# Kernel tuning notes

Measured on AMD Instinct MI355X. Metric: run time of the kernel, lower is better.

Reference implementation:

```python
import jax, jax.numpy as jnp
import numpy as np

N = 1024       # sentence length (words incl. root at index 0)
WD = 300       # word embedding dim (GloVe-style)
PD = 25        # pos_emb_dim
H = 125        # hidden_dim_lstm
FC = 100       # hidden_dim_fc
PVOCAB = 50    # POS tagset size


def setup_inputs() -> dict:
    key = jax.random.key(0)
    ks = jax.random.split(key, 14)
    f = lambda k, s: jax.random.normal(k, s, dtype=jnp.float32) * 0.1
    d_in = WD + PD
    return {
        "word_vecs": jax.random.normal(ks[0], (N, WD), dtype=jnp.float32),
        "pos_idx": jax.random.randint(ks[1], (N,), 0, PVOCAB),
        "parents_ids": jax.random.randint(ks[2], (N,), 0, N),
        "pos_emb": f(ks[3], (PVOCAB, PD)),
        "Wih0": f(ks[4], (2, 4 * H, d_in)),
        "Whh0": f(ks[5], (2, 4 * H, H)),
        "b0": f(ks[6], (2, 4 * H)),
        "Wih1": f(ks[7], (2, 4 * H, 2 * H)),
        "Whh1": f(ks[8], (2, 4 * H, H)),
        "b1": f(ks[9], (2, 4 * H)),
        "fc1_W": f(ks[10], (FC, 4 * H)),
        "fc1_b": f(ks[11], (FC,)),
        "fc2_W": f(ks[12], (1, FC)),
        "fc2_b": f(ks[13], (1,)),
    }


def _lstm_dir(x, Wih, Whh, b, reverse):
    # torch LSTM cell, gate order (i, f, g, o); b = b_ih + b_hh
    Hd = Whh.shape[1]
    def step(carry, xt):
        h, c = carry
        g = xt @ Wih.T + h @ Whh.T + b
        i, fg, gg, o = jnp.split(g, 4)
        i = jax.nn.sigmoid(i)
        fg = jax.nn.sigmoid(fg)
        gg = jnp.tanh(gg)
        o = jax.nn.sigmoid(o)
        c = fg * c + i * gg
        h = o * jnp.tanh(c)
        return (h, c), h
    init = (jnp.zeros((Hd,), x.dtype), jnp.zeros((Hd,), x.dtype))
    _, hs = jax.lax.scan(step, init, x, reverse=reverse)
    return hs  # [n, H], already in original time order


def _bilstm_layer(x, Wih, Whh, b):
    hf = _lstm_dir(x, Wih[0], Whh[0], b[0], False)
    hb = _lstm_dir(x, Wih[1], Whh[1], b[1], True)
    return jnp.concatenate([hf, hb], axis=1)  # [n, 2H]


def reference(word_vecs, pos_idx, parents_ids, pos_emb, Wih0, Whh0, b0,
              Wih1, Whh1, b1, fc1_W, fc1_b, fc2_W, fc2_b):
    # encoder: concat word + pos embeddings, 2-layer BiLSTM
    x = jnp.concatenate([word_vecs, pos_emb[pos_idx]], axis=1)  # [n, WD+PD]
    h = _bilstm_layer(x, Wih0, Whh0, b0)
    h = _bilstm_layer(h, Wih1, Whh1, b1)  # [n, 2H]
    n = h.shape[0]
    twoH = h.shape[1]
    # fc1(cat(h_i, h_j)) = h_i @ W_head^T + h_j @ W_child^T + b  (vectorized over all pairs)
    A = h @ fc1_W[:, :twoH].T   # head contribution  [n, FC]
    B = h @ fc1_W[:, twoH:].T   # child contribution [n, FC]
    T = jnp.tanh(A[:, None, :] + B[None, :, :] + fc1_b)  # [n, n, FC]
    raw = T @ fc2_W[0] + fc2_b[0]                         # [n, n]
    ii = jnp.arange(n)
    # original loop skips diagonal and arcs into the root (j == 0); those stay 0
    mask = (ii[:, None] != ii[None, :]) & (ii[None, :] != 0)
    scores_mat = jnp.where(mask, raw, jnp.float32(0.0))
    logits = scores_mat.T  # row j = scores of heads for child j
    logp = jax.nn.log_softmax(logits, axis=1)
    loss = -jnp.mean(logp[jnp.arange(n), parents_ids])
    return loss, scores_mat
```

## Files before the change

### kernel.cpp

```cpp
#include <hip/hip_runtime.h>

typedef float v2f __attribute__((ext_vector_type(2)));

#define LOG2E 1.4426950408889634f
#define LN2   0.6931471805599453f

__device__ __forceinline__ float fexp2(float x) {
  float r; asm("v_exp_f32 %0, %1" : "=v"(r) : "v"(x)); return r;
}
__device__ __forceinline__ float frcp(float x) {
  float r; asm("v_rcp_f32 %0, %1" : "=v"(r) : "v"(x)); return r;
}
__device__ __forceinline__ float flog2(float x) {
  float r; asm("v_log_f32 %0, %1" : "=v"(r) : "v"(x)); return r;
}
__device__ __forceinline__ float dpp_xor1(float v) {
  return __builtin_bit_cast(float,
      __builtin_amdgcn_update_dpp(0, __builtin_bit_cast(int, v), 0xB1, 0xF, 0xF, true));
}
__device__ __forceinline__ float dpp_xor2(float v) {
  return __builtin_bit_cast(float,
      __builtin_amdgcn_update_dpp(0, __builtin_bit_cast(int, v), 0x4E, 0xF, 0xF, true));
}
__device__ __forceinline__ void lgkm_barrier() {
  __builtin_amdgcn_sched_barrier(0);
  asm volatile("s_waitcnt lgkmcnt(0)" ::: "memory");
  __builtin_amdgcn_s_barrier();
  __builtin_amdgcn_sched_barrier(0);
}

__global__ void k_embed(const float* __restrict__ wv, const int* __restrict__ pidx,
                        const float* __restrict__ pemb, float* __restrict__ X) {
  int t = blockIdx.x;
  int pi = pidx[t];
  for (int c = threadIdx.x; c < 336; c += 128) {
    float v;
    if (c < 300)      v = wv[t * 300 + c];
    else if (c < 325) v = pemb[pi * 25 + (c - 300)];
    else              v = 0.f;
    X[t * 336 + c] = v;
  }
}

__global__ void k_repack(const float* __restrict__ src, float* __restrict__ dst,
                         int sK, int dK) {
  int r = blockIdx.x;
  for (int c = threadIdx.x; c < dK; c += 128)
    dst[r * dK + c] = (c < sK) ? src[r * sK + c] : 0.f;
}

__global__ void k_wab(const float* __restrict__ fc1W, float* __restrict__ Wab) {
  int r = blockIdx.x;
  int sr = (r < 100) ? r : r - 100;
  int so = (r < 100) ? 0 : 250;
  for (int c = threadIdx.x; c < 256; c += 128)
    Wab[r * 256 + c] = (c < 250) ? fc1W[sr * 500 + so + c] : 0.f;
}

__global__ void k_misc(const float* __restrict__ fc1b, const float* __restrict__ fc2W,
                       float* __restrict__ biasAB, float* __restrict__ sumw) {
  __shared__ float red[128];
  int t = threadIdx.x;
  for (int c = t; c < 256; c += 128)
    biasAB[c] = (c < 100) ? fc1b[c] : 0.f;
  float s = (t < 100) ? fc2W[t] : 0.f;
  red[t] = s; __syncthreads();
  for (int off = 64; off; off >>= 1) {
    if (t < off) red[t] += red[t + off];
    __syncthreads();
  }
  if (t == 0) sumw[0] = red[0];
}

#define BM 64
#define BN 64
#define BKK 16
__global__ __launch_bounds__(256) void k_gemm(
    const float* __restrict__ A, const float* __restrict__ Bw,
    const float* __restrict__ bias, float* __restrict__ C,
    int M, int N, int K, int ldC, long sBz, long sCz, long sbz, int transOut) {
  const int z = blockIdx.z;
  const float* Bp = Bw + (size_t)z * sBz;
  const float* bp = bias + (size_t)z * sbz;
  float* Cp = C + (size_t)z * sCz;
  const int bm = blockIdx.y * BM, bn = blockIdx.x * BN;
  __shared__ __align__(16) float As[BKK][BM + 4];
  __shared__ __align__(16) float Bs[BKK][BN + 4];
  __shared__ float Ts[BN][BM + 1];
  const int tid = threadIdx.x;
  const int tx = tid & 15, ty = tid >> 4;
  const int lr = tid >> 2;
  const int lk = (tid & 3) * 4;
  float acc[4][4];
#pragma unroll
  for (int a = 0; a < 4; ++a)
#pragma unroll
    for (int b = 0; b < 4; ++b) acc[a][b] = 0.f;

  int brow = bn + lr; if (brow >= N) brow = N - 1;
  for (int k0 = 0; k0 < K; k0 += BKK) {
    float4 a4 = *(const float4*)(A + (size_t)(bm + lr) * K + k0 + lk);
    float4 b4 = *(const float4*)(Bp + (size_t)brow * K + k0 + lk);
    __syncthreads();
    As[lk + 0][lr] = a4.x; As[lk + 1][lr] = a4.y; As[lk + 2][lr] = a4.z; As[lk + 3][lr] = a4.w;
    Bs[lk + 0][lr] = b4.x; Bs[lk + 1][lr] = b4.y; Bs[lk + 2][lr] = b4.z; Bs[lk + 3][lr] = b4.w;
    __syncthreads();
#pragma unroll
    for (int kk = 0; kk < BKK; ++kk) {
      float4 av = *(const float4*)&As[kk][ty * 4];
      float4 bv = *(const float4*)&Bs[kk][tx * 4];
      float aa[4] = {av.x, av.y, av.z, av.w};
      float bb[4] = {bv.x, bv.y, bv.z, bv.w};
#pragma unroll
      for (int a = 0; a < 4; ++a)
#pragma unroll
        for (int b = 0; b < 4; ++b)
          acc[a][b] = __builtin_fmaf(aa[a], bb[b], acc[a][b]);
    }
  }
  if (!transOut) {
#pragma unroll
    for (int a = 0; a < 4; ++a) {
      int i = bm + ty * 4 + a;
#pragma unroll
      for (int b = 0; b < 4; ++b) {
        int j = bn + tx * 4 + b;
        if (j < N) Cp[(size_t)i * ldC + j] = acc[a][b] + bp[j];
      }
    }
  } else {
    __syncthreads();
#pragma unroll
    for (int a = 0; a < 4; ++a)
#pragma unroll
      for (int b = 0; b < 4; ++b) {
        int jn = bn + tx * 4 + b; if (jn >= N) jn = N - 1;
        Ts[tx * 4 + b][ty * 4 + a] = acc[a][b] + bp[jn];
      }
    __syncthreads();
    const int n2 = tid >> 2, mq = (tid & 3) * 16;
    const int n = bn + n2;
    if (n < N) {
#pragma unroll
      for (int r = 0; r < 4; ++r) {
        int m0 = mq + r * 4;
        float4 v;
        v.x = Ts[n2][m0 + 0]; v.y = Ts[n2][m0 + 1];
        v.z = Ts[n2][m0 + 2]; v.w = Ts[n2][m0 + 3];
        *(float4*)(Cp + (size_t)n * ldC + bm + m0) = v;
      }
    }
  }
}

__global__ __launch_bounds__(512) void k_rec(const float* __restrict__ Pt,
                                             const float* __restrict__ Whh,
                                             float* __restrict__ hout) {
  const int d = blockIdx.x;
  const bool fwd = (d == 0);
  const int t = threadIdx.x;
  int u = t >> 2; const bool active = (u < 125); if (u > 124) u = 124;
  const int sub = t & 3;

  const float* Wd = Whh + (size_t)d * 500 * 125;
  v2f w[4][16];
#pragma unroll
  for (int g = 0; g < 4; ++g) {
    const float* wr = Wd + (size_t)(g * 125 + u) * 125;
#pragma unroll
    for (int j = 0; j < 16; ++j) {
      int col = sub * 32 + 2 * j;
      v2f ww;
      ww.x = (col     < 125) ? wr[col]     : 0.f;
      ww.y = (col + 1 < 125) ? wr[col + 1] : 0.f;
      w[g][j] = ww;
    }
  }

  __shared__ __align__(16) float hb[2][160];
  __shared__ float hist[32][128];
  for (int i = t; i < 320; i += 512) ((float*)hb)[i] = 0.f;

  const int prow = sub * 125 + u;
  const float4* Pr = (const float4*)(Pt + (size_t)d * 500 * 1024 + (size_t)prow * 1024);

  const float sM = (sub == 2) ? 2.f : 1.f;
  const float sA = (sub == 2) ? 2.f : 1.f;
  const float sB = (sub == 2) ? -1.f : 0.f;
  const bool m0s = (sub == 0), m1s = (sub == 1), m2s = (sub == 2);

  float cst = 0.f;
  float4 cura = Pr[fwd ? 0 : 254];
  float4 curb = Pr[fwd ? 1 : 255];
  __syncthreads();

  for (int cb = 0; cb < 128; ++cb) {
    int nc = (cb + 1 < 128) ? cb + 1 : cb;
    float4 nxta = Pr[fwd ? 2 * nc     : 254 - 2 * nc];
    float4 nxtb = Pr[fwd ? 2 * nc + 1 : 255 - 2 * nc];
#pragma unroll
    for (int e = 0; e < 8; ++e) {
      const int buf = e & 1;
      float pf = (e == 0) ? cura.x : (e == 1) ? cura.y : (e == 2) ? cura.z : (e == 3) ? cura.w
               : (e == 4) ? curb.x : (e == 5) ? curb.y : (e == 6) ? curb.z : curb.w;
      float pb = (e == 0) ? curb.w : (e == 1) ? curb.z : (e == 2) ? curb.y : (e == 3) ? curb.x
               : (e == 4) ? cura.w : (e == 5) ? cura.z : (e == 6) ? cura.y : cura.x;
      float pre = fwd ? pf : pb;
      const float4* hp = (const float4*)&hb[buf][36 * sub];
      v2f a0 = {0.f, 0.f}, a1 = {0.f, 0.f}, a2 = {0.f, 0.f}, a3 = {0.f, 0.f};
#pragma unroll
      for (int q = 0; q < 8; ++q) {
        float4 hv = hp[q];
        v2f ha; ha.x = hv.x; ha.y = hv.y;
        v2f hc; hc.x = hv.z; hc.y = hv.w;
        a0 = __builtin_elementwise_fma(w[0][2 * q], ha, a0);
        a0 = __builtin_elementwise_fma(w[0][2 * q + 1], hc, a0);
        a1 = __builtin_elementwise_fma(w[1][2 * q], ha, a1);
        a1 = __builtin_elementwise_fma(w[1][2 * q + 1], hc, a1);
        a2 = __builtin_elementwise_fma(w[2][2 * q], ha, a2);
        a2 = __builtin_elementwise_fma(w[2][2 * q + 1], hc, a2);
        a3 = __builtin_elementwise_fma(w[3][2 * q], ha, a3);
        a3 = __builtin_elementwise_fma(w[3][2 * q + 1], hc, a3);
      }
      float p0 = a0.x + a0.y, p1 = a1.x + a1.y, p2 = a2.x + a2.y, p3 = a3.x + a3.y;
      p0 += dpp_xor1(p0); p0 += dpp_xor2(p0);
      p1 += dpp_xor1(p1); p1 += dpp_xor2(p1);
      p2 += dpp_xor1(p2); p2 += dpp_xor2(p2);
      p3 += dpp_xor1(p3); p3 += dpp_xor2(p3);
      float x = m0s ? p0 : m1s ? p1 : m2s ? p2 : p3;
      x += pre;
      float sg = frcp(1.f + fexp2(-LOG2E * (sM * x)));
      float a = __builtin_fmaf(sA, sg, sB);
      float fg = dpp_xor1(a);
      float gg = dpp_xor2(a);
      float og = dpp_xor2(fg);
      cst = __builtin_fmaf(fg, cst, a * gg);
      float th = __builtin_fmaf(2.f, frcp(1.f + fexp2(-2.f * LOG2E * cst)), -1.f);
      float h = og * th;
      if (m0s && active) {
        hb[buf ^ 1][u + 4 * (u >> 5)] = h;
        hist[(cb & 3) * 8 + e][u] = h;
      }
      lgkm_barrier();
    }
    if ((cb & 3) == 3) {
      const int S0 = (cb - 3) * 8;
#pragma unroll
      for (int k = 0; k < 8; ++k) {
        int idx = t + k * 512;
        int r = idx >> 7, u2 = idx & 127;
        if (u2 < 125) {
          int step = S0 + r;
          int time = fwd ? step : 1023 - step;
          hout[(size_t)time * 256 + d * 125 + u2] = hist[r][u2];
        }
      }
      lgkm_barrier();
    }
    cura = nxta; curb = nxtb;
  }
}

__global__ __launch_bounds__(256) void k_pair(const float* __restrict__ AB,
    const float* __restrict__ fc2W, const float* __restrict__ fc2b,
    const float* __restrict__ sumw, float* __restrict__ outS,
    float* __restrict__ scoresT) {
  __shared__ float As[32][100];
  __shared__ float Bs[32][101];
  __shared__ float w2s[100];
  const int tid = threadIdx.x;
  const int i0 = blockIdx.y * 32, j0 = blockIdx.x * 32;
  for (int idx = tid; idx < 3200; idx += 256) {
    int r = idx / 100, k = idx - r * 100;
    As[r][k] = AB[(size_t)(i0 + r) * 200 + k];
    Bs[r][k] = AB[(size_t)(j0 + r) * 200 + 100 + k];
  }
  if (tid < 100) w2s[tid] = 2.f * fc2W[tid];
  __syncthreads();
  const int tx = tid & 31, ty = tid >> 5;
  float acc[4] = {0.f, 0.f, 0.f, 0.f};
#pragma unroll 4
  for (int k = 0; k < 100; ++k) {
    float b = Bs[tx][k];
    float wk2 = w2s[k];
    float bs = b * (2.f * LOG2E);
#pragma unroll
    for (int q = 0; q < 4; ++q) {
      float a = As[ty + 8 * q][k];
      float r = frcp(1.f + fexp2(__builtin_fmaf(a, 2.f * LOG2E, bs)));
      acc[q] = __builtin_fmaf(wk2, r, acc[q]);
    }
  }
  float base = sumw[0] + fc2b[0];
  const int j = j0 + tx;
#pragma unroll
  for (int q = 0; q < 4; ++q) {
    int i = i0 + ty + 8 * q;
    float val = (i != j && j != 0) ? (base - acc[q]) : 0.f;
    outS[(size_t)i * 1024 + j] = val;
    scoresT[(size_t)j * 1024 + i] = val;
  }
}

__global__ __launch_bounds__(256) void k_soft(const float* __restrict__ scoresT,
    const int* __restrict__ parents, float* __restrict__ contrib) {
  const int j = blockIdx.x, tid = threadIdx.x;
  __shared__ float red[256];
  const float* row = scoresT + (size_t)j * 1024;
  float v0 = row[tid], v1 = row[tid + 256], v2 = row[tid + 512], v3 = row[tid + 768];
  float m = fmaxf(fmaxf(v0, v1), fmaxf(v2, v3));
  red[tid] = m; __syncthreads();
  for (int off = 128; off; off >>= 1) {
    if (tid < off) red[tid] = fmaxf(red[tid], red[tid + off]);
    __syncthreads();
  }
  m = red[0]; __syncthreads();
  float s = fexp2((v0 - m) * LOG2E) + fexp2((v1 - m) * LOG2E) +
            fexp2((v2 - m) * LOG2E) + fexp2((v3 - m) * LOG2E);
  red[tid] = s; __syncthreads();
  for (int off = 128; off; off >>= 1) {
    if (tid < off) red[tid] += red[tid + off];
    __syncthreads();
  }
  if (tid == 0) {
    float S = red[0];
    int p = parents[j];
    contrib[j] = row[p] - m - flog2(S) * LN2;
  }
}

__global__ __launch_bounds__(256) void k_loss(const float* __restrict__ contrib,
                                              float* __restrict__ out) {
  __shared__ float red[256];
  int tid = threadIdx.x;
  float s = contrib[tid] + contrib[tid + 256] + contrib[tid + 512] + contrib[tid + 768];
  red[tid] = s; __syncthreads();
  for (int off = 128; off; off >>= 1) {
    if (tid < off) red[tid] += red[tid + off];
    __syncthreads();
  }
  if (tid == 0) out[0] = -red[0] * (1.f / 1024.f);
}

extern "C" void kernel_launch(void* const* d_in, const int* in_sizes, int n_in,
                              void* d_out, int out_size, void* d_ws, size_t ws_size,
                              hipStream_t stream) {
  const float* wv   = (const float*)d_in[0];
  const int*   pidx = (const int*)d_in[1];
  const int*   par  = (const int*)d_in[2];
  const float* pemb = (const float*)d_in[3];
  const float* Wih0 = (const float*)d_in[4];
  const float* Whh0 = (const float*)d_in[5];
  const float* b0   = (const float*)d_in[6];
  const float* Wih1 = (const float*)d_in[7];
  const float* Whh1 = (const float*)d_in[8];
  const float* b1   = (const float*)d_in[9];
  const float* fc1W = (const float*)d_in[10];
  const float* fc1b = (const float*)d_in[11];
  const float* fc2W = (const float*)d_in[12];
  const float* fc2b = (const float*)d_in[13];
  float* ws = (float*)d_ws;
  float* X      = ws + 0;
  float* Wih0p  = ws + 344064;
  float* Pt0    = ws + 680064;
  float* h0     = ws + 1704064;
  float* Wih1p  = ws + 1966208;
  float* Pt1    = ws + 2222208;
  float* h1     = ws + 3246208;
  float* Wab    = ws + 3508352;
  float* biasAB = ws + 3559552;
  float* AB     = ws + 3559808;
  float* scT    = ws + 3764608;
  float* contrib= ws + 4813184;
  float* sumw   = ws + 4814208;
  float* out = (float*)d_out;

  hipMemsetAsync(h0, 0, 1024 * 256 * sizeof(float), stream);
  hipMemsetAsync(h1, 0, 1024 * 256 * sizeof(float), stream);

  k_embed <<<1024, 128, 0, stream>>>(wv, pidx, pemb, X);
  k_repack<<<1000, 128, 0, stream>>>(Wih0, Wih0p, 325, 336);
  k_repack<<<1000, 128, 0, stream>>>(Wih1, Wih1p, 250, 256);
  k_wab   <<<200, 128, 0, stream>>>(fc1W, Wab);
  k_misc  <<<1, 128, 0, stream>>>(fc1b, fc2W, biasAB, sumw);

  k_gemm<<<dim3(8, 16, 2), 256, 0, stream>>>(X, Wih0p, b0, Pt0, 1024, 500, 336, 1024,
                                             500L * 336, 500L * 1024, 500L, 1);
  k_rec <<<2, 512, 0, stream>>>(Pt0, Whh0, h0);
  k_gemm<<<dim3(8, 16, 2), 256, 0, stream>>>(h0, Wih1p, b1, Pt1, 1024, 500, 256, 1024,
                                             500L * 256, 500L * 1024, 500L, 1);
  k_rec <<<2, 512, 0, stream>>>(Pt1, Whh1, h1);
  k_gemm<<<dim3(4, 16, 1), 256, 0, stream>>>(h1, Wab, biasAB, AB, 1024, 200, 256, 200,
                                             0L, 0L, 0L, 0);
  k_pair<<<dim3(32, 32), 256, 0, stream>>>(AB, fc2W, fc2b, sumw, out + 1, scT);
  k_soft<<<1024, 256, 0, stream>>>(scT, par, contrib);
  k_loss<<<1, 256, 0, stream>>>(contrib, out);
}
```

Baseline: 1.328 ms.

## Compute LSTM recurrent matvec with fp16 MFMA instead of FP32 FMA

Replaces the per-thread FP32 FMA recurrent matvec plus DPP reductions in the recurrence kernel with 16x16x32 fp16 MFMA instructions. Weights are held as fp16 fragments and hidden state is stored in LDS as fp16. Each lane now computes all four gates for one unit directly, and the input projection is staged through LDS as the accumulator initialiser. This should shorten the per-timestep serial critical path, at the cost of fp16 rounding of weights and hidden state, which may hurt accuracy over 1024 steps.

Result: faster. 1.212 ms (-8.7%).

```diff
diff --git a/kernel.cpp b/kernel.cpp
--- a/kernel.cpp
+++ b/kernel.cpp
@@ -1,6 +1,8 @@
 #include <hip/hip_runtime.h>
 
 typedef float v2f __attribute__((ext_vector_type(2)));
+typedef _Float16 f16x8 __attribute__((ext_vector_type(8)));
+typedef float f32x4 __attribute__((ext_vector_type(4)));
 
 #define LOG2E 1.4426950408889634f
 #define LN2   0.6931471805599453f
@@ -13,14 +15,6 @@
 }
 __device__ __forceinline__ float flog2(float x) {
   float r; asm("v_log_f32 %0, %1" : "=v"(r) : "v"(x)); return r;
-}
-__device__ __forceinline__ float dpp_xor1(float v) {
-  return __builtin_bit_cast(float,
-      __builtin_amdgcn_update_dpp(0, __builtin_bit_cast(int, v), 0xB1, 0xF, 0xF, true));
-}
-__device__ __forceinline__ float dpp_xor2(float v) {
-  return __builtin_bit_cast(float,
-      __builtin_amdgcn_update_dpp(0, __builtin_bit_cast(int, v), 0x4E, 0xF, 0xF, true));
 }
 __device__ __forceinline__ void lgkm_barrier() {
   __builtin_amdgcn_sched_barrier(0);
@@ -159,88 +153,92 @@
   const int d = blockIdx.x;
   const bool fwd = (d == 0);
   const int t = threadIdx.x;
-  int u = t >> 2; const bool active = (u < 125); if (u > 124) u = 124;
+  const int w  = t >> 6;
+  const int l  = t & 63;
+  const int lg = l >> 4;
+  const int lc = l & 15;
+  const int q  = lc >> 2;
+
+  int u_p = t >> 2; const bool activep = (u_p < 125); if (u_p > 124) u_p = 124;
   const int sub = t & 3;
+  const float4* Pr = (const float4*)(Pt + (size_t)d * 500 * 1024 +
+                                     (size_t)(sub * 125 + u_p) * 1024);
 
   const float* Wd = Whh + (size_t)d * 500 * 125;
-  v2f w[4][16];
-#pragma unroll
-  for (int g = 0; g < 4; ++g) {
-    const float* wr = Wd + (size_t)(g * 125 + u) * 125;
-#pragma unroll
-    for (int j = 0; j < 16; ++j) {
-      int col = sub * 32 + 2 * j;
-      v2f ww;
-      ww.x = (col     < 125) ? wr[col]     : 0.f;
-      ww.y = (col + 1 < 125) ? wr[col + 1] : 0.f;
-      w[g][j] = ww;
-    }
-  }
-
-  __shared__ __align__(16) float hb[2][160];
+  f16x8 a[4][4];
+#pragma unroll
+  for (int rt = 0; rt < 4; ++rt) {
+    const int rho = (w << 6) + (rt << 4) + lc;
+    const int u2 = rho >> 2, g2 = rho & 3;
+    const bool uok = (u2 < 125);
+    const float* wr2 = Wd + (size_t)(g2 * 125 + (uok ? u2 : 0)) * 125;
+#pragma unroll
+    for (int kt = 0; kt < 4; ++kt) {
+      f16x8 v;
+#pragma unroll
+      for (int j = 0; j < 8; ++j) {
+        const int k = kt * 32 + lg * 8 + j;
+        v[j] = (_Float16)((uok && k < 125) ? wr2[k] : 0.f);
+      }
+      a[rt][kt] = v;
+    }
+  }
+
+  __shared__ __align__(16) _Float16 hf[2][128];
+  __shared__ __align__(16) float preb[2][512];
   __shared__ float hist[32][128];
-  for (int i = t; i < 320; i += 512) ((float*)hb)[i] = 0.f;
-
-  const int prow = sub * 125 + u;
-  const float4* Pr = (const float4*)(Pt + (size_t)d * 500 * 1024 + (size_t)prow * 1024);
-
-  const float sM = (sub == 2) ? 2.f : 1.f;
-  const float sA = (sub == 2) ? 2.f : 1.f;
-  const float sB = (sub == 2) ? -1.f : 0.f;
-  const bool m0s = (sub == 0), m1s = (sub == 1), m2s = (sub == 2);
-
-  float cst = 0.f;
+  for (int i = t; i < 128; i += 512) ((int*)hf)[i] = 0;
+  for (int i = t; i < 1024; i += 512) ((float*)preb)[i] = 0.f;
+
   float4 cura = Pr[fwd ? 0 : 254];
   float4 curb = Pr[fwd ? 1 : 255];
+  float cst = 0.f;
+  if (activep) preb[0][t] = fwd ? cura.x : curb.w;
   __syncthreads();
 
   for (int cb = 0; cb < 128; ++cb) {
-    int nc = (cb + 1 < 128) ? cb + 1 : cb;
+    const int nc = (cb + 1 < 128) ? cb + 1 : cb;
     float4 nxta = Pr[fwd ? 2 * nc     : 254 - 2 * nc];
     float4 nxtb = Pr[fwd ? 2 * nc + 1 : 255 - 2 * nc];
 #pragma unroll
     for (int e = 0; e < 8; ++e) {
       const int buf = e & 1;
-      float pf = (e == 0) ? cura.x : (e == 1) ? cura.y : (e == 2) ? cura.z : (e == 3) ? cura.w
-               : (e == 4) ? curb.x : (e == 5) ? curb.y : (e == 6) ? curb.z : curb.w;
-      float pb = (e == 0) ? curb.w : (e == 1) ? curb.z : (e == 2) ? curb.y : (e == 3) ? curb.x
-               : (e == 4) ? cura.w : (e == 5) ? cura.z : (e == 6) ? cura.y : cura.x;
-      float pre = fwd ? pf : pb;
-      const float4* hp = (const float4*)&hb[buf][36 * sub];
-      v2f a0 = {0.f, 0.f}, a1 = {0.f, 0.f}, a2 = {0.f, 0.f}, a3 = {0.f, 0.f};
-#pragma unroll
-      for (int q = 0; q < 8; ++q) {
-        float4 hv = hp[q];
-        v2f ha; ha.x = hv.x; ha.y = hv.y;
-        v2f hc; hc.x = hv.z; hc.y = hv.w;
-        a0 = __builtin_elementwise_fma(w[0][2 * q], ha, a0);
-        a0 = __builtin_elementwise_fma(w[0][2 * q + 1], hc, a0);
-        a1 = __builtin_elementwise_fma(w[1][2 * q], ha, a1);
-        a1 = __builtin_elementwise_fma(w[1][2 * q + 1], hc, a1);
-        a2 = __builtin_elementwise_fma(w[2][2 * q], ha, a2);
-        a2 = __builtin_elementwise_fma(w[2][2 * q + 1], hc, a2);
-        a3 = __builtin_elementwise_fma(w[3][2 * q], ha, a3);
-        a3 = __builtin_elementwise_fma(w[3][2 * q + 1], hc, a3);
-      }
-      float p0 = a0.x + a0.y, p1 = a1.x + a1.y, p2 = a2.x + a2.y, p3 = a3.x + a3.y;
-      p0 += dpp_xor1(p0); p0 += dpp_xor2(p0);
-      p1 += dpp_xor1(p1); p1 += dpp_xor2(p1);
-      p2 += dpp_xor1(p2); p2 += dpp_xor2(p2);
-      p3 += dpp_xor1(p3); p3 += dpp_xor2(p3);
-      float x = m0s ? p0 : m1s ? p1 : m2s ? p2 : p3;
-      x += pre;
-      float sg = frcp(1.f + fexp2(-LOG2E * (sM * x)));
-      float a = __builtin_fmaf(sA, sg, sB);
-      float fg = dpp_xor1(a);
-      float gg = dpp_xor2(a);
-      float og = dpp_xor2(fg);
-      cst = __builtin_fmaf(fg, cst, a * gg);
+      f16x8 hfr[4];
+#pragma unroll
+      for (int kt = 0; kt < 4; ++kt)
+        hfr[kt] = *(const f16x8*)&hf[buf][kt * 32 + lg * 8];
+      f32x4 acc[4];
+#pragma unroll
+      for (int rt = 0; rt < 4; ++rt)
+        acc[rt] = *(const f32x4*)&preb[buf][(w << 6) + (rt << 4) + (lg << 2)];
+#pragma unroll
+      for (int kt = 0; kt < 4; ++kt)
+#pragma unroll
+        for (int rt = 0; rt < 4; ++rt)
+          acc[rt] = __builtin_amdgcn_mfma_f32_16x16x32_f16(a[rt][kt], hfr[kt],
+                                                           acc[rt], 0, 0, 0);
+      f32x4 T = (q == 0) ? acc[0] : (q == 1) ? acc[1] : (q == 2) ? acc[2] : acc[3];
+      float gi = frcp(1.f + fexp2(-LOG2E * T[0]));
+      float gf = frcp(1.f + fexp2(-LOG2E * T[1]));
+      float gg = __builtin_fmaf(2.f, frcp(1.f + fexp2(-2.f * LOG2E * T[2])), -1.f);
+      float go = frcp(1.f + fexp2(-LOG2E * T[3]));
+      cst = __builtin_fmaf(gf, cst, gi * gg);
       float th = __builtin_fmaf(2.f, frcp(1.f + fexp2(-2.f * LOG2E * cst)), -1.f);
-      float h = og * th;
-      if (m0s && active) {
-        hb[buf ^ 1][u + 4 * (u >> 5)] = h;
-        hist[(cb & 3) * 8 + e][u] = h;
-      }
+      float hv = go * th;
+      float pf, pb2;
+      if (e < 7) {
+        pf  = (e == 0) ? cura.y : (e == 1) ? cura.z : (e == 2) ? cura.w
+            : (e == 3) ? curb.x : (e == 4) ? curb.y : (e == 5) ? curb.z : curb.w;
+        pb2 = (e == 0) ? curb.z : (e == 1) ? curb.y : (e == 2) ? curb.x
+            : (e == 3) ? cura.w : (e == 4) ? cura.z : (e == 5) ? cura.y : cura.x;
+      } else { pf = nxta.x; pb2 = nxtb.w; }
+      const float pre_next = fwd ? pf : pb2;
+      const int u_own = (w << 4) + (q << 2) + lg;
+      if (((lc & 3) == 0) && u_own < 125) {
+        hf[buf ^ 1][u_own] = (_Float16)hv;
+        hist[(cb & 3) * 8 + e][u_own] = hv;
+      }
+      if (activep) preb[buf ^ 1][t] = pre_next;
       lgkm_barrier();
     }
     if ((cb & 3) == 3) {
```
